# Kernel tuning notes

Measured on AMD Instinct MI355X. Metric: run time of the kernel, lower is better.

Reference implementation:

```python
import jax, jax.numpy as jnp
import numpy as np
from jax.ops import segment_sum

N_NODES, N_EDGES, FEAT, HID, LAT = 50000, 800000, 128, 64, 32
NUM_GRAPHS, MAX_NODES = 64, 30


def setup_inputs() -> dict:
    key = jax.random.key(0)
    ks = jax.random.split(key, 24)
    def lin(k, fi, fo):
        kw, kb = jax.random.split(k)
        s = 1.0 / np.sqrt(fi)
        return (jax.random.uniform(kw, (fi, fo), jnp.float32, -s, s),
                jax.random.uniform(kb, (fo,), jnp.float32, -s, s))
    W1, b1 = lin(ks[0], FEAT, HID)
    W2, b2 = lin(ks[1], HID, HID)
    Wmu, bmu = lin(ks[2], HID, LAT)
    Wlv, blv = lin(ks[3], HID, LAT)
    Wl1, bl1 = lin(ks[4], LAT, HID)
    Wl2, bl2 = lin(ks[5], HID, HID * MAX_NODES)
    We1, be1 = lin(ks[6], 2 * HID, HID)
    We2, be2 = lin(ks[7], HID, 1)
    x = jax.random.normal(ks[8], (N_NODES, FEAT), jnp.float32)
    edge_index = jax.random.randint(ks[9], (2, N_EDGES), 0, N_NODES, jnp.int64)
    batch = jnp.sort(jax.random.randint(ks[10], (N_NODES,), 0, NUM_GRAPHS, jnp.int64))
    return {"x": x, "edge_index": edge_index, "batch": batch, "num_nodes": MAX_NODES,
            "W1": W1, "b1": b1, "W2": W2, "b2": b2, "Wmu": Wmu, "bmu": bmu,
            "Wlv": Wlv, "blv": blv, "Wl1": Wl1, "bl1": bl1, "Wl2": Wl2, "bl2": bl2,
            "We1": We1, "be1": be1, "We2": We2, "be2": be2}


def reference(x, edge_index, batch, num_nodes, W1, b1, W2, b2, Wmu, bmu,
              Wlv, blv, Wl1, bl1, Wl2, bl2, We1, be1, We2, be2):
    N = x.shape[0]
    src, dst = edge_index[0], edge_index[1]
    # GCN normalization with self-loops: deg over A+I
    deg = segment_sum(jnp.ones_like(src, jnp.float32), dst, num_segments=N) + 1.0
    dinv = jax.lax.rsqrt(deg)
    enorm = dinv[src] * dinv[dst]            # [E]
    snorm = dinv * dinv                      # self-loop norm [N]

    def gcn(h, W, b):
        h = h @ W                            # transform before gather (smaller)
        agg = segment_sum(h[src] * enorm[:, None], dst, num_segments=N)
        return agg + h * snorm[:, None] + b

    h = jax.nn.relu(gcn(x, W1, b1))
    h = jax.nn.relu(gcn(h, W2, b2))

    counts = segment_sum(jnp.ones((N,), jnp.float32), batch, num_segments=NUM_GRAPHS)
    pooled = segment_sum(h, batch, num_segments=NUM_GRAPHS) / jnp.maximum(counts, 1.0)[:, None]
    mu = pooled @ Wmu + bmu
    logvar = pooled @ Wlv + blv
    z = mu  # eval-mode reparameterize

    node_emb = (jax.nn.relu(z @ Wl1 + bl1) @ Wl2 + bl2).reshape(NUM_GRAPHS, MAX_NODES, HID)
    emb = node_emb[0, :num_nodes]            # [n, HID]
    Wtop, Wbot = We1[:HID], We1[HID:]
    hi = emb @ Wtop                          # [n, HID]
    hj = emb @ Wbot
    hidp = jax.nn.relu(hi[:, None, :] + hj[None, :, :] + be1)  # [n, n, HID]
    probs = jax.nn.sigmoid((hidp @ We2)[..., 0] + be2[0])       # [n, n]
    upper = jnp.triu(probs, k=1)
    adj = upper + upper.T
    return adj, mu, logvar
```

## Files before the change

### kernel.cpp

```cpp
#include <hip/hip_runtime.h>
#include <hip/hip_bf16.h>
#include <math.h>

#define FEAT 128
#define HID 64
#define LAT 32
#define NG 64
#define MAXN 30
#define NPART 8
#define CAP 64
#define T_OCT 655
#define FILL_OCT 262

typedef __hip_bfloat16 bf16;
typedef short bf16x8 __attribute__((ext_vector_type(8)));
typedef float f32x4 __attribute__((ext_vector_type(4)));

__global__ void k_zero_conv(int* p, int nzero, int zb,
                            const float* __restrict__ W1,
                            const float* __restrict__ W2,
                            bf16* __restrict__ w1t,
                            bf16* __restrict__ w2t) {
    int tid = threadIdx.x;
    if ((int)blockIdx.x < zb) {
        int i = blockIdx.x * 256 + tid;
        if (i < nzero) p[i] = 0;
        return;
    }
    int idx = (blockIdx.x - zb) * 256 + tid;
    if (idx < FEAT * HID) {
        int k = idx >> 6, f = idx & 63;
        w1t[f * FEAT + k] = __float2bfloat16(W1[idx]);
    } else if (idx < FEAT * HID + HID * HID) {
        int r = idx - FEAT * HID;
        int k = r >> 6, f = r & 63;
        w2t[f * HID + k] = __float2bfloat16(W2[r]);
    }
}

__global__ __launch_bounds__(256) void k_fill_gemm(const int* __restrict__ src,
                                                   const int* __restrict__ dst,
                                                   int* __restrict__ cnt,
                                                   unsigned short* __restrict__ slots,
                                                   const float* __restrict__ x,
                                                   const bf16* __restrict__ w1t,
                                                   bf16* __restrict__ hw,
                                                   int N, int E) {
    __shared__ __align__(16) bf16 X[16][136];
    int tid = threadIdx.x;
    int o = blockIdx.x >> 3;
    int xcd = blockIdx.x & 7;
    if (o % 5 < 2) {
        int bi = (o / 5) * 2 + (o % 5);
        int psz0 = (N + NPART - 1) / NPART;
        int base = xcd * psz0;
        int psize = min(psz0, N - base);
        const long stride = (long)FILL_OCT * 256;
        for (long e = (long)bi * 256 + tid; e < E; e += stride) {
            int d = dst[e];
            int r = d - base;
            if ((unsigned)r < (unsigned)psize) {
                int pos = atomicAdd(&cnt[d], 1);
                if (pos < CAP) slots[((long)d << 6) + pos] = (unsigned short)src[e];
            }
        }
        return;
    }
    int go = (o / 5) * 3 + (o % 5) - 2;
    int gblk = go * 8 + xcd;
    if (gblk >= (N + 15) / 16) return;
    int r0 = gblk * 16;
    {
        int kw = tid & 63;
        int rr = tid >> 6;
        for (int r = rr; r < 16; r += 4) {
            int row = r0 + r;
            float x0 = 0.f, x1 = 0.f;
            if (row < N) {
                const float* xp = x + (long)row * FEAT + 2 * kw;
                x0 = xp[0];
                x1 = xp[1];
            }
            __hip_bfloat162 p;
            p.x = __float2bfloat16(x0);
            p.y = __float2bfloat16(x1);
            *(__hip_bfloat162*)&X[r][2 * kw] = p;
        }
    }
    __syncthreads();
    int wv = tid >> 6, lane = tid & 63;
    int m = lane & 15;
    int kb = (lane >> 4) * 8;
    int f0 = wv * 16;
    const bf16* wrow = w1t + (f0 + m) * FEAT;
    f32x4 acc = {0.f, 0.f, 0.f, 0.f};
#pragma unroll
    for (int t = 0; t < 4; ++t) {
        bf16x8 a = *reinterpret_cast<const bf16x8*>(&X[m][kb + 32 * t]);
        bf16x8 bb = *reinterpret_cast<const bf16x8*>(wrow + kb + 32 * t);
        acc = __builtin_amdgcn_mfma_f32_16x16x32_bf16(a, bb, acc, 0, 0, 0);
    }
#pragma unroll
    for (int rg = 0; rg < 4; ++rg) {
        int row = (lane >> 4) * 4 + rg;
        int nid = r0 + row;
        if (nid < N) hw[((long)nid << 6) + f0 + m] = __float2bfloat16(acc[rg]);
    }
}

__device__ inline void red4(float4& a) {
    a.x += __shfl_xor(a.x, 16); a.y += __shfl_xor(a.y, 16);
    a.z += __shfl_xor(a.z, 16); a.w += __shfl_xor(a.w, 16);
    a.x += __shfl_xor(a.x, 32); a.y += __shfl_xor(a.y, 32);
    a.z += __shfl_xor(a.z, 32); a.w += __shfl_xor(a.w, 32);
}

#define ACC4(v, en)                                              \
    acc.x += __uint_as_float(((v).x & 0xFFFFu) << 16) * (en);    \
    acc.y += __uint_as_float((v).x & 0xFFFF0000u) * (en);        \
    acc.z += __uint_as_float(((v).y & 0xFFFFu) << 16) * (en);    \
    acc.w += __uint_as_float((v).y & 0xFFFF0000u) * (en);

__device__ inline float4 gather_core(const bf16* __restrict__ hw,
                                     const unsigned short* __restrict__ slots,
                                     const int* __restrict__ cnt,
                                     int wid, int cntv, float di, int lane,
                                     const float* __restrict__ b) {
    int sub = lane >> 4, q = lane & 15;
    long j0 = (long)wid << 6;
    float4 acc = make_float4(0.f, 0.f, 0.f, 0.f);
    int s_r = wid;
    float en_r = 0.0f;
    if (lane < cntv) {
        s_r = slots[j0 + lane];
        en_r = rsqrtf(1.0f + (float)cnt[s_r]) * di;
    }
    int nld = (cntv + 3) >> 2;
    uint2 v[16];
#pragma unroll
    for (int l = 0; l < 16; ++l) {
        if (l < nld) {
            int s = __shfl(s_r, l * 4 + sub);
            v[l] = *reinterpret_cast<const uint2*>(hw + (((long)s << 6) + (q << 2)));
        }
    }
#pragma unroll
    for (int l = 0; l < 16; ++l) {
        if (l < nld) {
            float en = __shfl(en_r, l * 4 + sub);
            ACC4(v[l], en);
        }
    }
    red4(acc);
    uint2 sv = *reinterpret_cast<const uint2*>(hw + (((long)wid << 6) + (q << 2)));
    float sn = di * di;
    float4 bq = *reinterpret_cast<const float4*>(b + (q << 2));
    acc.x += __uint_as_float((sv.x & 0xFFFFu) << 16) * sn + bq.x;
    acc.y += __uint_as_float(sv.x & 0xFFFF0000u) * sn + bq.y;
    acc.z += __uint_as_float((sv.y & 0xFFFFu) << 16) * sn + bq.z;
    acc.w += __uint_as_float(sv.y & 0xFFFF0000u) * sn + bq.w;
    return acc;
}

__global__ __launch_bounds__(1024) void k_gather_mm(const bf16* __restrict__ hw,
                                                    const unsigned short* __restrict__ slots,
                                                    const int* __restrict__ cnt,
                                                    const float* __restrict__ b1,
                                                    const bf16* __restrict__ w2t,
                                                    bf16* __restrict__ hw2, int N) {
    __shared__ __align__(16) bf16 H[16][72];
    int tid = threadIdx.x;
    int wv = tid >> 6, lane = tid & 63;
    int wid = blockIdx.x * 16 + wv;
    if (wid < N) {
        int c_full = cnt[wid];
        int cntv = min(c_full, CAP);
        float di = rsqrtf(1.0f + (float)c_full);
        float4 r = gather_core(hw, slots, cnt, wid, cntv, di, lane, b1);
        if (lane < 16) {
            int c = lane << 2;
            H[wv][c + 0] = __float2bfloat16(fmaxf(r.x, 0.f));
            H[wv][c + 1] = __float2bfloat16(fmaxf(r.y, 0.f));
            H[wv][c + 2] = __float2bfloat16(fmaxf(r.z, 0.f));
            H[wv][c + 3] = __float2bfloat16(fmaxf(r.w, 0.f));
        }
    }
    __syncthreads();
    if (wv < 4) {
        int m = lane & 15;
        int kb = (lane >> 4) * 8;
        int f0 = wv * 16;
        const bf16* wrow = w2t + (f0 + m) * HID;
        bf16x8 a0 = *reinterpret_cast<const bf16x8*>(&H[m][kb]);
        bf16x8 a1 = *reinterpret_cast<const bf16x8*>(&H[m][kb + 32]);
        bf16x8 b0 = *reinterpret_cast<const bf16x8*>(wrow + kb);
        bf16x8 b1f = *reinterpret_cast<const bf16x8*>(wrow + kb + 32);
        f32x4 acc = {0.f, 0.f, 0.f, 0.f};
        acc = __builtin_amdgcn_mfma_f32_16x16x32_bf16(a0, b0, acc, 0, 0, 0);
        acc = __builtin_amdgcn_mfma_f32_16x16x32_bf16(a1, b1f, acc, 0, 0, 0);
#pragma unroll
        for (int rg = 0; rg < 4; ++rg) {
            int row = (lane >> 4) * 4 + rg;
            int nid = blockIdx.x * 16 + row;
            if (nid < N) hw2[((long)nid << 6) + f0 + m] = __float2bfloat16(acc[rg]);
        }
    }
}

__global__ __launch_bounds__(256) void k_gather4(const bf16* __restrict__ hw,
                                                 const unsigned short* __restrict__ slots,
                                                 const int* __restrict__ cnt,
                                                 const float* __restrict__ b,
                                                 float* __restrict__ outb, int N) {
    int wv = threadIdx.x >> 6, lane = threadIdx.x & 63;
    int wid = blockIdx.x * 4 + wv;
    if (wid >= N) return;
    int c_full = cnt[wid];
    int cntv = min(c_full, CAP);
    float di = rsqrtf(1.0f + (float)c_full);
    float4 r = gather_core(hw, slots, cnt, wid, cntv, di, lane, b);
    if ((lane >> 4) == 0)
        *reinterpret_cast<float4*>(outb + (((long)wid << 6) + ((lane & 15) << 2))) = r;
}

__global__ __launch_bounds__(256) void k_relu_pool(const float* __restrict__ agg,
                                                   const int* __restrict__ batch,
                                                   float* __restrict__ pooled,
                                                   float* __restrict__ counts,
                                                   int N, int rows_per_wave) {
    int wid = blockIdx.x * (blockDim.x >> 6) + (threadIdx.x >> 6);
    int lane = threadIdx.x & 63;
    int i0 = wid * rows_per_wave;
    if (i0 >= N) return;
    int i1 = min(i0 + rows_per_wave, N);
    int cur = batch[i0];
    float acc = 0.0f, cnt = 0.0f;
    for (int i = i0; i < i1; ++i) {
        int g = batch[i];
        if (g != cur) {
            atomicAdd(&pooled[cur * 64 + lane], acc);
            if (lane == 0) atomicAdd(&counts[cur], cnt);
            acc = 0.0f; cnt = 0.0f; cur = g;
        }
        acc += fmaxf(agg[(long)i * 64 + lane], 0.0f);
        cnt += 1.0f;
    }
    atomicAdd(&pooled[cur * 64 + lane], acc);
    if (lane == 0) atomicAdd(&counts[cur], cnt);
}

__global__ __launch_bounds__(256) void k_heads_dec1(const float* __restrict__ pooled,
                                                    const float* __restrict__ counts,
                                                    const float* __restrict__ Wmu,
                                                    const float* __restrict__ bmu,
                                                    const float* __restrict__ Wlv,
                                                    const float* __restrict__ blv,
                                                    const float* __restrict__ Wl1,
                                                    const float* __restrict__ bl1,
                                                    const float* __restrict__ Wl2,
                                                    const float* __restrict__ bl2,
                                                    const float* __restrict__ We1,
                                                    float* __restrict__ out,
                                                    float* __restrict__ hi,
                                                    float* __restrict__ hj) {
    int blk = blockIdx.x;
    int tid = threadIdx.x;
    if (blk < MAXN) {
        __shared__ float prow[HID];
        __shared__ float z0[LAT];
        __shared__ float hr[HID];
        __shared__ float em[HID];
        int n = blk;
        if (tid < HID) prow[tid] = pooled[tid];
        __syncthreads();
        if (tid < LAT) {
            float c0 = fmaxf(counts[0], 1.0f);
            float s = 0.0f;
#pragma unroll 8
            for (int h = 0; h < HID; ++h) s += prow[h] * Wmu[h * 32 + tid];
            z0[tid] = s / c0 + bmu[tid];
        }
        __syncthreads();
        if (tid < HID) {
            float s = bl1[tid];
#pragma unroll
            for (int l = 0; l < LAT; ++l) s += z0[l] * Wl1[l * HID + tid];
            hr[tid] = fmaxf(s, 0.0f);
        }
        __syncthreads();
        if (tid < HID) {
            float e = bl2[n * HID + tid];
#pragma unroll 8
            for (int h = 0; h < HID; ++h) e += hr[h] * Wl2[h * (HID * MAXN) + n * HID + tid];
            em[tid] = e;
        }
        __syncthreads();
        if (tid < HID) {
            float a = 0.0f, bb = 0.0f;
#pragma unroll 8
            for (int f = 0; f < HID; ++f) {
                float ev = em[f];
                a += ev * We1[f * HID + tid];
                bb += ev * We1[(HID + f) * HID + tid];
            }
            hi[n * HID + tid] = a;
            hj[n * HID + tid] = bb;
        }
    } else {
        int idx = (blk - MAXN) * 256 + tid;
        int which = idx >> 11;
        int r = idx & (NG * LAT - 1);
        int g = r >> 5, l = r & 31;
        const float* W = which ? Wlv : Wmu;
        const float* b = which ? blv : bmu;
        float s = 0.0f;
#pragma unroll 8
        for (int h = 0; h < HID; ++h) s += pooled[g * 64 + h] * W[h * 32 + l];
        float c = fmaxf(counts[g], 1.0f);
        out[900 + idx] = s / c + b[l];
    }
}

__global__ __launch_bounds__(256) void k_dec2(const float* __restrict__ hi,
                                              const float* __restrict__ hj,
                                              const float* __restrict__ be1,
                                              const float* __restrict__ We2,
                                              const float* __restrict__ be2,
                                              float* __restrict__ out) {
    __shared__ float shi[MAXN * 65];
    __shared__ float shj[MAXN * 65];
    __shared__ float sbe[HID];
    __shared__ float sw[HID];
    int tid = threadIdx.x;
    for (int i = tid; i < MAXN * HID; i += 256) {
        int n = i >> 6, k = i & 63;
        shi[n * 65 + k] = hi[i];
        shj[n * 65 + k] = hj[i];
    }
    if (tid < HID) { sbe[tid] = be1[tid]; sw[tid] = We2[tid]; }
    __syncthreads();
    float bias2 = be2[0];
    for (int idx = tid; idx < MAXN * MAXN; idx += 256) {
        int i = idx / MAXN, j = idx % MAXN;
        if (i == j) { out[idx] = 0.0f; continue; }
        int a = i < j ? i : j;
        int b = i < j ? j : i;
        float s = bias2;
#pragma unroll 8
        for (int k = 0; k < HID; ++k)
            s += fmaxf(shi[a * 65 + k] + shj[b * 65 + k] + sbe[k], 0.0f) * sw[k];
        out[idx] = 1.0f / (1.0f + expf(-s));
    }
}

extern "C" void kernel_launch(void* const* d_in, const int* in_sizes, int n_in,
                              void* d_out, int out_size, void* d_ws, size_t ws_size,
                              hipStream_t stream) {
    const float* x = (const float*)d_in[0];
    const int* ei = (const int*)d_in[1];
    const int* batch = (const int*)d_in[2];
    const float* W1 = (const float*)d_in[4];
    const float* b1 = (const float*)d_in[5];
    const float* W2 = (const float*)d_in[6];
    const float* b2 = (const float*)d_in[7];
    const float* Wmu = (const float*)d_in[8];
    const float* bmu = (const float*)d_in[9];
    const float* Wlv = (const float*)d_in[10];
    const float* blv = (const float*)d_in[11];
    const float* Wl1 = (const float*)d_in[12];
    const float* bl1 = (const float*)d_in[13];
    const float* Wl2 = (const float*)d_in[14];
    const float* bl2 = (const float*)d_in[15];
    const float* We1 = (const float*)d_in[16];
    const float* be1 = (const float*)d_in[17];
    const float* We2 = (const float*)d_in[18];
    const float* be2 = (const float*)d_in[19];

    const int N = in_sizes[2];
    const int E = in_sizes[1] / 2;
    const int* src = ei;
    const int* dst = ei + E;

    char* ws = (char*)d_ws;
    size_t off_b = 0;
    auto alloc = [&](size_t nbytes) {
        void* p = (void*)(ws + off_b);
        off_b = (off_b + nbytes + 255) & ~(size_t)255;
        return p;
    };
    float* bufA   = (float*)alloc((size_t)N * 64 * 4);
    bf16*  hwb1   = (bf16*)alloc((size_t)N * 64 * 2);
    bf16*  hwb2   = (bf16*)alloc((size_t)N * 64 * 2);
    const int nzero = N + NG * HID + NG;
    int*   cnt    = (int*)alloc((size_t)nzero * 4);
    float* pooled = (float*)(cnt + N);
    float* counts = pooled + NG * HID;
    unsigned short* slots = (unsigned short*)alloc((size_t)N * CAP * 2);
    bf16*  w1t    = (bf16*)alloc(FEAT * HID * 2);
    bf16*  w2t    = (bf16*)alloc(HID * HID * 2);
    float* dhi    = (float*)alloc(MAXN * HID * 4);
    float* dhj    = (float*)alloc(MAXN * HID * 4);

    float* out = (float*)d_out;

    const int zb = (nzero + 255) / 256;
    const int cvb = (FEAT * HID + HID * HID + 255) / 256;
    k_zero_conv<<<zb + cvb, 256, 0, stream>>>(cnt, nzero, zb, W1, W2, w1t, w2t);

    k_fill_gemm<<<T_OCT * 8, 256, 0, stream>>>(src, dst, cnt, slots,
                                               x, w1t, hwb1, N, E);

    k_gather_mm<<<(N + 15) / 16, 1024, 0, stream>>>(hwb1, slots, cnt, b1, w2t, hwb2, N);

    k_gather4<<<(N + 3) / 4, 256, 0, stream>>>(hwb2, slots, cnt, b2, bufA, N);

    {
        const int waves = 2048;
        int rpw = (N + waves - 1) / waves;
        k_relu_pool<<<512, 256, 0, stream>>>(bufA, batch, pooled, counts, N, rpw);
    }

    k_heads_dec1<<<MAXN + 16, 256, 0, stream>>>(pooled, counts, Wmu, bmu, Wlv, blv,
                                                Wl1, bl1, Wl2, bl2, We1, out, dhi, dhj);

    k_dec2<<<1, 256, 0, stream>>>(dhi, dhj, be1, We2, be2, out);
}
```

Measured before the change: 140.6 us.

## Split edge adjacency into per-XCD private bucket lists with precomputed dinv

Replaces the dst-range partitioned fill, where every fill block scans all edges and keeps only its partition, with per-XCD private count and slot arrays. Each edge is now read exactly once, and atomics stay local to one XCD's copy. The gather merges the 8 sub-lists per node: it compacts valid lanes with ballot and ds_permute, then runs two load rounds. A new small kernel precomputes dinv from the summed counts so the gathers do not recompute rsqrt. In exchange the gather does extra compaction work and reads 8x the count array, and the per-partition cap of 16 can drop edges on skewed inputs.

```diff
diff --git a/kernel.cpp b/kernel.cpp
--- a/kernel.cpp
+++ b/kernel.cpp
@@ -8,9 +8,10 @@
 #define NG 64
 #define MAXN 30
 #define NPART 8
-#define CAP 64
+#define CAPP 16
 #define T_OCT 655
 #define FILL_OCT 262
+#define FILL_BLOCKS (FILL_OCT * 8)
 
 typedef __hip_bfloat16 bf16;
 typedef short bf16x8 __attribute__((ext_vector_type(8)));
@@ -40,8 +41,8 @@
 
 __global__ __launch_bounds__(256) void k_fill_gemm(const int* __restrict__ src,
                                                    const int* __restrict__ dst,
-                                                   int* __restrict__ cnt,
-                                                   unsigned short* __restrict__ slots,
+                                                   int* __restrict__ cnt8,
+                                                   unsigned short* __restrict__ slots8,
                                                    const float* __restrict__ x,
                                                    const bf16* __restrict__ w1t,
                                                    bf16* __restrict__ hw,
@@ -51,18 +52,15 @@
     int o = blockIdx.x >> 3;
     int xcd = blockIdx.x & 7;
     if (o % 5 < 2) {
-        int bi = (o / 5) * 2 + (o % 5);
-        int psz0 = (N + NPART - 1) / NPART;
-        int base = xcd * psz0;
-        int psize = min(psz0, N - base);
-        const long stride = (long)FILL_OCT * 256;
-        for (long e = (long)bi * 256 + tid; e < E; e += stride) {
+        int fo = (o / 5) * 2 + (o % 5);
+        long fb = (long)fo * 8 + xcd;
+        int* mycnt = cnt8 + (size_t)xcd * N;
+        unsigned short* mysl = slots8 + (size_t)xcd * N * CAPP;
+        const long stride = (long)FILL_BLOCKS * 256;
+        for (long e = fb * 256 + tid; e < E; e += stride) {
             int d = dst[e];
-            int r = d - base;
-            if ((unsigned)r < (unsigned)psize) {
-                int pos = atomicAdd(&cnt[d], 1);
-                if (pos < CAP) slots[((long)d << 6) + pos] = (unsigned short)src[e];
-            }
+            int pos = atomicAdd(&mycnt[d], 1);
+            if (pos < CAPP) mysl[(long)d * CAPP + pos] = (unsigned short)src[e];
         }
         return;
     }
@@ -108,6 +106,16 @@
     }
 }
 
+__global__ void k_dinv8(const int* __restrict__ cnt8, float* __restrict__ dinv, int N) {
+    int i = blockIdx.x * 256 + threadIdx.x;
+    if (i < N) {
+        int s = 0;
+#pragma unroll
+        for (int p = 0; p < 8; ++p) s += cnt8[(size_t)p * N + i];
+        dinv[i] = rsqrtf(1.0f + (float)s);
+    }
+}
+
 __device__ inline void red4(float4& a) {
     a.x += __shfl_xor(a.x, 16); a.y += __shfl_xor(a.y, 16);
     a.z += __shfl_xor(a.z, 16); a.w += __shfl_xor(a.w, 16);
@@ -121,34 +129,48 @@
     acc.z += __uint_as_float(((v).y & 0xFFFFu) << 16) * (en);    \
     acc.w += __uint_as_float((v).y & 0xFFFF0000u) * (en);
 
-__device__ inline float4 gather_core(const bf16* __restrict__ hw,
-                                     const unsigned short* __restrict__ slots,
-                                     const int* __restrict__ cnt,
-                                     int wid, int cntv, float di, int lane,
-                                     const float* __restrict__ b) {
+__device__ inline float4 gather_core8(const bf16* __restrict__ hw,
+                                      const unsigned short* __restrict__ slots8,
+                                      const int* __restrict__ cnt8,
+                                      const float* __restrict__ dinv,
+                                      int wid, float di, int lane,
+                                      const float* __restrict__ b, int N) {
     int sub = lane >> 4, q = lane & 15;
-    long j0 = (long)wid << 6;
     float4 acc = make_float4(0.f, 0.f, 0.f, 0.f);
-    int s_r = wid;
-    float en_r = 0.0f;
-    if (lane < cntv) {
-        s_r = slots[j0 + lane];
-        en_r = rsqrtf(1.0f + (float)cnt[s_r]) * di;
-    }
-    int nld = (cntv + 3) >> 2;
-    uint2 v[16];
-#pragma unroll
-    for (int l = 0; l < 16; ++l) {
-        if (l < nld) {
-            int s = __shfl(s_r, l * 4 + sub);
-            v[l] = *reinterpret_cast<const uint2*>(hw + (((long)s << 6) + (q << 2)));
-        }
-    }
-#pragma unroll
-    for (int l = 0; l < 16; ++l) {
-        if (l < nld) {
-            float en = __shfl(en_r, l * 4 + sub);
-            ACC4(v[l], en);
+#pragma unroll
+    for (int r = 0; r < 2; ++r) {
+        int p = (lane >> 4) + r * 4;
+        int c = cnt8[(size_t)p * N + wid];
+        int j = lane & 15;
+        bool valid = j < c;
+        int s = wid;
+        float en = 0.0f;
+        if (valid) {
+            s = slots8[((size_t)p * N + wid) * CAPP + j];
+            en = dinv[s] * di;
+        }
+        unsigned long long mask = __ballot(valid);
+        int tot = __popcll(mask);
+        int below = __popcll(mask & ((1ull << lane) - 1ull));
+        int tgt = valid ? below : (tot + lane - below);
+        int s_c = __builtin_amdgcn_ds_permute(tgt << 2, s);
+        float en_c = __int_as_float(
+            __builtin_amdgcn_ds_permute(tgt << 2, __float_as_int(en)));
+        int nld = (tot + 3) >> 2;
+        uint2 v[16];
+#pragma unroll
+        for (int l = 0; l < 16; ++l) {
+            if (l < nld) {
+                int ss = __shfl(s_c, l * 4 + sub);
+                v[l] = *reinterpret_cast<const uint2*>(hw + (((long)ss << 6) + (q << 2)));
+            }
+        }
+#pragma unroll
+        for (int l = 0; l < 16; ++l) {
+            if (l < nld) {
+                float ee = __shfl(en_c, l * 4 + sub);
+                ACC4(v[l], ee);
+            }
         }
     }
     red4(acc);
@@ -163,8 +185,9 @@
 }
 
 __global__ __launch_bounds__(1024) void k_gather_mm(const bf16* __restrict__ hw,
-                                                    const unsigned short* __restrict__ slots,
-                                                    const int* __restrict__ cnt,
+                                                    const unsigned short* __restrict__ slots8,
+                                                    const int* __restrict__ cnt8,
+                                                    const float* __restrict__ dinv,
                                                     const float* __restrict__ b1,
                                                     const bf16* __restrict__ w2t,
                                                     bf16* __restrict__ hw2, int N) {
@@ -173,10 +196,8 @@
     int wv = tid >> 6, lane = tid & 63;
     int wid = blockIdx.x * 16 + wv;
     if (wid < N) {
-        int c_full = cnt[wid];
-        int cntv = min(c_full, CAP);
-        float di = rsqrtf(1.0f + (float)c_full);
-        float4 r = gather_core(hw, slots, cnt, wid, cntv, di, lane, b1);
+        float di = dinv[wid];
+        float4 r = gather_core8(hw, slots8, cnt8, dinv, wid, di, lane, b1, N);
         if (lane < 16) {
             int c = lane << 2;
             H[wv][c + 0] = __float2bfloat16(fmaxf(r.x, 0.f));
@@ -208,17 +229,16 @@
 }
 
 __global__ __launch_bounds__(256) void k_gather4(const bf16* __restrict__ hw,
-                                                 const unsigned short* __restrict__ slots,
-                                                 const int* __restrict__ cnt,
+                                                 const unsigned short* __restrict__ slots8,
+                                                 const int* __restrict__ cnt8,
+                                                 const float* __restrict__ dinv,
                                                  const float* __restrict__ b,
                                                  float* __restrict__ outb, int N) {
     int wv = threadIdx.x >> 6, lane = threadIdx.x & 63;
     int wid = blockIdx.x * 4 + wv;
     if (wid >= N) return;
-    int c_full = cnt[wid];
-    int cntv = min(c_full, CAP);
-    float di = rsqrtf(1.0f + (float)c_full);
-    float4 r = gather_core(hw, slots, cnt, wid, cntv, di, lane, b);
+    float di = dinv[wid];
+    float4 r = gather_core8(hw, slots8, cnt8, dinv, wid, di, lane, b, N);
     if ((lane >> 4) == 0)
         *reinterpret_cast<float4*>(outb + (((long)wid << 6) + ((lane & 15) << 2))) = r;
 }
@@ -391,11 +411,12 @@
     float* bufA   = (float*)alloc((size_t)N * 64 * 4);
     bf16*  hwb1   = (bf16*)alloc((size_t)N * 64 * 2);
     bf16*  hwb2   = (bf16*)alloc((size_t)N * 64 * 2);
-    const int nzero = N + NG * HID + NG;
-    int*   cnt    = (int*)alloc((size_t)nzero * 4);
-    float* pooled = (float*)(cnt + N);
+    float* dinv   = (float*)alloc((size_t)N * 4);
+    const int nzero = 8 * N + NG * HID + NG;
+    int*   cnt8   = (int*)alloc((size_t)nzero * 4);
+    float* pooled = (float*)(cnt8 + 8 * N);
     float* counts = pooled + NG * HID;
-    unsigned short* slots = (unsigned short*)alloc((size_t)N * CAP * 2);
+    unsigned short* slots8 = (unsigned short*)alloc((size_t)8 * N * CAPP * 2);
     bf16*  w1t    = (bf16*)alloc(FEAT * HID * 2);
     bf16*  w2t    = (bf16*)alloc(HID * HID * 2);
     float* dhi    = (float*)alloc(MAXN * HID * 4);
@@ -405,14 +426,16 @@
 
     const int zb = (nzero + 255) / 256;
     const int cvb = (FEAT * HID + HID * HID + 255) / 256;
-    k_zero_conv<<<zb + cvb, 256, 0, stream>>>(cnt, nzero, zb, W1, W2, w1t, w2t);
-
-    k_fill_gemm<<<T_OCT * 8, 256, 0, stream>>>(src, dst, cnt, slots,
+    k_zero_conv<<<zb + cvb, 256, 0, stream>>>(cnt8, nzero, zb, W1, W2, w1t, w2t);
+
+    k_fill_gemm<<<T_OCT * 8, 256, 0, stream>>>(src, dst, cnt8, slots8,
                                                x, w1t, hwb1, N, E);
 
-    k_gather_mm<<<(N + 15) / 16, 1024, 0, stream>>>(hwb1, slots, cnt, b1, w2t, hwb2, N);
-
-    k_gather4<<<(N + 3) / 4, 256, 0, stream>>>(hwb2, slots, cnt, b2, bufA, N);
+    k_dinv8<<<(N + 255) / 256, 256, 0, stream>>>(cnt8, dinv, N);
+
+    k_gather_mm<<<(N + 15) / 16, 1024, 0, stream>>>(hwb1, slots8, cnt8, dinv, b1, w2t, hwb2, N);
+
+    k_gather4<<<(N + 3) / 4, 256, 0, stream>>>(hwb2, slots8, cnt8, dinv, b2, bufA, N);
 
     {
         const int waves = 2048;
```

Result: slower. 207.2 us (+47.4%).
